# Kernel tuning notes

Hardware: AMD Instinct MI355X
Metric: run time of the kernel (lower is better)

Reference implementation:

```python
import jax, jax.numpy as jnp
import numpy as np

T_STEPS = 128
N_RAYS = 16384
RAY_EXT = 10.0  # ray_ext_factor


def _posenc(x, n_freq=4):
    # x: (...,3) in [-1,1] -> (...,3 + 3*2*n_freq) = (...,27)
    feats = [x]
    for k in range(n_freq):
        f = (2.0 ** k) * jnp.pi
        feats.append(jnp.sin(f * x))
        feats.append(jnp.cos(f * x))
    return jnp.concatenate(feats, -1)


def _sh_deg2(d):
    # real spherical harmonics, degree 0 and 1 (4 coeffs), d unit vectors (...,3)
    x, y, z = d[..., 0], d[..., 1], d[..., 2]
    c0 = 0.28209479177387814
    c1 = 0.4886025119029199
    return jnp.stack([jnp.full_like(x, c0), c1 * y, c1 * z, c1 * x], -1)


def _forward(rays_o, rays_d, tnoise, aabb, W1, b1, W2, b2, Wc1, bc1, Wc2, bc2):
    # --- ray-AABB intersection (slab method), RayBundle.intersect_aabb ---
    inv_d = 1.0 / rays_d
    t0 = (aabb[0] - rays_o) * inv_d
    t1 = (aabb[1] - rays_o) * inv_d
    tnear = jnp.maximum(jnp.max(jnp.minimum(t0, t1), -1, keepdims=True), 0.0)  # (N,1)
    tfar = jnp.min(jnp.maximum(t0, t1), -1, keepdims=True)                      # (N,1)
    active = (tfar > tnear).astype(rays_o.dtype)  # active_mask; masking replaces compaction

    # --- StratifiedRayStepSampler: ts (T,N,1) ---
    T = tnoise.shape[0]
    base = (jnp.arange(T, dtype=rays_o.dtype)[:, None, None] + tnoise) / T
    ts = tnear[None] + (tfar - tnear)[None] * base
    xyz = rays_o[None] + ts * rays_d[None]  # (T,N,3)

    # --- vol.sample(xyz, ynm, return_color=True): density + color MLP ---
    xn = 2.0 * (xyz - aabb[0]) / (aabb[1] - aabb[0]) - 1.0
    enc = _posenc(xn)                             # (T,N,27)
    h = jax.nn.relu(enc @ W1 + b1)                # (T,N,64)
    dh = h @ W2 + b2                              # (T,N,16)
    sigma = jnp.exp(dh[..., :1])                  # (T,N,1) density
    feat = dh[..., 1:]                            # (T,N,15)
    dnorm = jnp.linalg.norm(rays_d, axis=-1, keepdims=True)  # (N,1)
    ynm = _sh_deg2(rays_d / dnorm)                # encode_raydir -> (N,4)
    ynm = jnp.broadcast_to(ynm[None], (T,) + ynm.shape)      # expand to (T,N,4)
    hc = jax.nn.relu(jnp.concatenate([feat, ynm], -1) @ Wc1 + bc1)
    rgb = jax.nn.sigmoid(hc @ Wc2 + bc2)          # (T,N,3)

    # --- integrate_timesteps: transmittance-weighted compositing ---
    tfinal = tfar * RAY_EXT
    delta = jnp.concatenate([ts[1:] - ts[:-1], tfinal[None] - ts[-1:]], 0)  # (T,N,1)
    sd = sigma * delta * dnorm[None]
    alpha = 1.0 - jnp.exp(-sd)
    trans = jnp.exp(-(jnp.cumsum(sd, 0) - sd))    # exclusive cumsum transmittance
    w = trans * alpha * active[None]              # (T,N,1); inactive rays -> zero maps

    color = jnp.sum(w * rgb, 0)                   # color_map  (N,3)
    alpha_map = jnp.sum(w, 0)                     # alpha_map  (N,1)
    return jnp.concatenate([color, alpha_map], -1)  # rgba (N,4)


def setup_inputs() -> dict:
    key = jax.random.key(0)
    ks = jax.random.split(key, 8)
    # origins on a sphere of radius 2.5 around the unit aabb, aimed at points inside it
    o = jax.random.normal(ks[0], (N_RAYS, 3), jnp.float32)
    o = 2.5 * o / jnp.linalg.norm(o, axis=-1, keepdims=True)
    tgt = jax.random.uniform(ks[1], (N_RAYS, 3), jnp.float32, -0.5, 0.5)
    d = tgt - o
    d = d / jnp.linalg.norm(d, axis=-1, keepdims=True)
    aabb = jnp.array([[-1.0, -1.0, -1.0], [1.0, 1.0, 1.0]], jnp.float32)
    tnoise = jax.random.uniform(ks[2], (T_STEPS, N_RAYS, 1), jnp.float32)
    s1, s2, s3, s4 = 27 ** -0.5, 64 ** -0.5, 19 ** -0.5, 64 ** -0.5
    return {
        'rays_o': o, 'rays_d': d, 'tnoise': tnoise, 'aabb': aabb,
        'W1': jax.random.normal(ks[3], (27, 64), jnp.float32) * s1,
        'b1': jnp.zeros((64,), jnp.float32),
        'W2': jax.random.normal(ks[4], (64, 16), jnp.float32) * (0.1 * s2),
        'b2': jnp.zeros((16,), jnp.float32),
        'Wc1': jax.random.normal(ks[5], (19, 64), jnp.float32) * s3,
        'bc1': jnp.zeros((64,), jnp.float32),
        'Wc2': jax.random.normal(ks[6], (64, 3), jnp.float32) * s4,
        'bc2': jnp.zeros((3,), jnp.float32),
    }


def reference(rays_o, rays_d, tnoise, aabb, W1, b1, W2, b2, Wc1, bc1, Wc2, bc2):
    return _forward(rays_o, rays_d, tnoise, aabb, W1, b1, W2, b2, Wc1, bc1, Wc2, bc2)
```

## Files before the change

### kernel.cpp

```cpp
#include <hip/hip_runtime.h>
#include <stdint.h>

#define N_RAYS  16384
#define T_STEPS 128
#define RPW   16
#define WAVES 8
#define TSEG  16

typedef _Float16 half8  __attribute__((ext_vector_type(8)));
typedef __fp16   fp16x2 __attribute__((ext_vector_type(2)));
typedef float    float4_ __attribute__((ext_vector_type(4)));
typedef uint32_t uint2_  __attribute__((ext_vector_type(2)));

#define H8_W1    0
#define H8_FUSED 256
#define H8_WC2   896
#define F32_CV   4096
#define F32_BC2  4416
#define F32_S0   4432

__device__ __forceinline__ uint32_t pk(float a, float b) {
    fp16x2 h = __builtin_amdgcn_cvt_pkrtz(a, b);
    return __builtin_bit_cast(uint32_t, h);
}
__device__ __forceinline__ uint32_t pkr(float a, float b) {
    fp16x2 h = __builtin_amdgcn_cvt_pkrtz(a, b);
    fp16x2 z = {(__fp16)0.f, (__fp16)0.f};
    fp16x2 m = __builtin_elementwise_max(h, z);
    return __builtin_bit_cast(uint32_t, m);
}

__global__ void prep_weights(const float* __restrict__ W1, const float* __restrict__ b1,
                             const float* __restrict__ W2, const float* __restrict__ b2,
                             const float* __restrict__ Wc1, const float* __restrict__ bc1,
                             const float* __restrict__ Wc2, const float* __restrict__ bc2,
                             void* __restrict__ ws) {
    _Float16* wh = (_Float16*)ws;
    float*    wf = (float*)ws;
    int frag = blockIdx.x;
    int lane = threadIdx.x;
    int mm = lane & 15, q = lane >> 4;
    if (frag < 4) {
        int tau = frag;
        int n = tau * 16 + mm;
        for (int j = 0; j < 8; ++j) {
            float w;
            if (j < 6)      w = W1[(3 + 6 * q + j) * 64 + n];
            else if (j == 6) w = (q == 0) ? W1[0 * 64 + n] : (q == 1) ? W1[2 * 64 + n] : 0.f;
            else             w = (q == 0) ? W1[1 * 64 + n] : (q == 1) ? b1[n] : 0.f;
            wh[(H8_W1 + tau * 64 + lane) * 8 + j] = (_Float16)w;
        }
    } else if (frag < 14) {
        int f = frag - 4;
        int tau = f >> 1, kap = f & 1;
        int n_out = tau * 16 + mm;
        for (int j = 0; j < 8; ++j) {
            int k = kap * 32 + q * 8 + j;
            float w = 0.f;
            if (n_out < 64) {
                for (int c = 0; c < 15; ++c)
                    w += W2[k * 16 + 1 + c] * Wc1[c * 64 + n_out];
            } else if (n_out == 64) {
                w = W2[k * 16 + 0];
            }
            wh[(H8_FUSED + f * 64 + lane) * 8 + j] = (_Float16)w;
        }
    } else {
        int kap = frag - 14;
        for (int j = 0; j < 8; ++j) {
            int k = kap * 32 + q * 8 + j;
            wh[(H8_WC2 + kap * 64 + lane) * 8 + j] =
                (_Float16)((mm < 3) ? Wc2[k * 3 + mm] : 0.f);
        }
        if (frag == 15) {
            int n = lane;
            wf[F32_CV + 0 * 64 + n] = Wc1[15 * 64 + n];
            wf[F32_CV + 1 * 64 + n] = Wc1[16 * 64 + n];
            wf[F32_CV + 2 * 64 + n] = Wc1[17 * 64 + n];
            wf[F32_CV + 3 * 64 + n] = Wc1[18 * 64 + n];
            float cc = bc1[n];
            for (int c = 0; c < 15; ++c) cc += b2[1 + c] * Wc1[c * 64 + n];
            wf[F32_CV + 4 * 64 + n] = cc;
            if (lane < 16) wf[F32_BC2 + lane] = (lane < 3) ? bc2[lane] : 0.f;
            if (lane == 0) wf[F32_S0] = b2[0];
        }
    }
}

__global__ __launch_bounds__(512, 3)
void render_kernel(const float* __restrict__ rays_o, const float* __restrict__ rays_d,
                   const float* __restrict__ tnoise, const float* __restrict__ aabb,
                   const void* __restrict__ ws, float* __restrict__ out) {
    __shared__ __align__(16) _Float16 sH[WAVES][2][1024];
    __shared__ float sComb[WAVES][RPW][5];

    const int tid  = threadIdx.x;
    const int wv   = tid >> 6;
    const int lane = tid & 63;
    const int m    = lane & 15;
    const int q    = lane >> 4;
    const int r    = blockIdx.x * RPW + m;

    const half8* wsv = (const half8*)ws;
    const float* wsf = (const float*)ws;
    half8 fW1[4], fF[10], fWc2[2];
    #pragma unroll
    for (int i = 0; i < 4; ++i)  fW1[i]  = wsv[H8_W1    + i * 64 + lane];
    #pragma unroll
    for (int i = 0; i < 10; ++i) fF[i]   = wsv[H8_FUSED + i * 64 + lane];
    #pragma unroll
    for (int i = 0; i < 2; ++i)  fWc2[i] = wsv[H8_WC2   + i * 64 + lane];
    const float4_ binit = ((const float4_*)(wsf + F32_BC2))[q];
    const float s0b = wsf[F32_S0];

    float o0 = rays_o[r * 3 + 0], o1 = rays_o[r * 3 + 1], o2 = rays_o[r * 3 + 2];
    float d0 = rays_d[r * 3 + 0], d1 = rays_d[r * 3 + 1], d2 = rays_d[r * 3 + 2];
    float a00 = aabb[0], a01 = aabb[1], a02 = aabb[2];
    float a10 = aabb[3], a11 = aabb[4], a12 = aabb[5];

    float i0 = 1.0f / d0, i1 = 1.0f / d1, i2 = 1.0f / d2;
    float u0 = (a00 - o0) * i0, v0 = (a10 - o0) * i0;
    float u1 = (a01 - o1) * i1, v1 = (a11 - o1) * i1;
    float u2 = (a02 - o2) * i2, v2 = (a12 - o2) * i2;
    float tnear = fmaxf(fmaxf(fmaxf(fminf(u0, v0), fminf(u1, v1)), fminf(u2, v2)), 0.0f);
    float tfar  = fminf(fminf(fmaxf(u0, v0), fmaxf(u1, v1)), fmaxf(u2, v2));
    bool active = (tfar > tnear);
    float dt = tfar - tnear;
    float dt128 = dt * (1.0f / 128.0f);

    float dn  = sqrtf(d0 * d0 + d1 * d1 + d2 * d2);
    float idn = 1.0f / dn;
    const float c0sh = 0.28209479177387814f;
    const float c1sh = 0.4886025119029199f;
    float y1 = c1sh * d1 * idn, y2 = c1sh * d2 * idn, y3 = c1sh * d0 * idn;

    float4_ cv[4];
    #pragma unroll
    for (int tau = 0; tau < 4; ++tau) {
        #pragma unroll
        for (int reg = 0; reg < 4; ++reg) {
            int n = tau * 16 + 4 * q + reg;
            float c = wsf[F32_CV + 4 * 64 + n];
            c = fmaf(c0sh, wsf[F32_CV + 0 * 64 + n], c);
            c = fmaf(y1,   wsf[F32_CV + 1 * 64 + n], c);
            c = fmaf(y2,   wsf[F32_CV + 2 * 64 + n], c);
            c = fmaf(y3,   wsf[F32_CV + 3 * 64 + n], c);
            cv[tau][reg] = c;
        }
    }
    const float4_ c4init = {s0b, s0b, s0b, s0b};

    float qs = 0.5f * (float)(1 << q);
    float sc0 = 2.0f / (a10 - a00), of0 = -a00 * sc0 - 1.0f;
    float sc1 = 2.0f / (a11 - a01), of1 = -a01 * sc1 - 1.0f;
    float sc2 = 2.0f / (a12 - a02), of2 = -a02 * sc2 - 1.0f;
    float scq0 = sc0 * qs, ofq0 = of0 * qs;
    float scq1 = sc1 * qs, ofq1 = of1 * qs;
    float scq2 = sc2 * qs, ofq2 = of2 * qs;

    _Float16*       hwp[2];
    const _Float16* hrp[2];
    #pragma unroll
    for (int p = 0; p < 2; ++p) {
        hwp[p] = &sH[wv][p][((q >> 1) * 16 + m) * 8 + 4 * (q & 1)];
        hrp[p] = &sH[wv][p][(q * 16 + m) * 8];
    }

    const float4_ z4 = {0.f, 0.f, 0.f, 0.f};
    const bool q0 = (q == 0), q1 = (q == 1);

    float trans = 1.0f, sdtot = 0.0f, wacc = 0.0f;
    float cacc0 = 0.0f, cacc1 = 0.0f, cacc2 = 0.0f;

    const int tbase = wv * TSEG;
    float nA = tnoise[(tbase + 0) * N_RAYS + r];
    float nB = tnoise[(tbase + 1) * N_RAYS + r];

    #pragma unroll 1
    for (int tt = 0; tt < TSEG; tt += 2) {
        const int t0 = tbase + tt, t1 = t0 + 1;
        float nC = (t0 + 2 < T_STEPS) ? tnoise[(t0 + 2) * N_RAYS + r] : 0.0f;
        float nD = (t0 + 3 < T_STEPS) ? tnoise[(t0 + 3) * N_RAYS + r] : 0.0f;
        float ts0 = fmaf((float)t0 + nA, dt128, tnear);
        float ts1 = fmaf((float)t1 + nB, dt128, tnear);
        float ts2 = fmaf((float)(t0 + 2) + nC, dt128, tnear);
        float tsP[2] = {ts0, ts1};
        float deltaP[2];
        deltaP[0] = ts1 - ts0;
        deltaP[1] = (t1 < T_STEPS - 1) ? (ts2 - ts1) : fmaf(tfar, 10.0f, -ts1);
        nA = nC; nB = nD;

        float dhx[2];
        float4_ rgbP[2];

        #pragma unroll
        for (int p = 0; p < 2; ++p) {
            float x = fmaf(tsP[p], d0, o0);
            float y = fmaf(tsP[p], d1, o1);
            float z = fmaf(tsP[p], d2, o2);
            float xr0 = fmaf(x, scq0, ofq0);
            float xr1 = fmaf(y, scq1, ofq1);
            float xr2 = fmaf(z, scq2, ofq2);
            float s0 = __builtin_amdgcn_sinf(xr0);
            float s1 = __builtin_amdgcn_sinf(xr1);
            float s2 = __builtin_amdgcn_sinf(xr2);
            float cA = __builtin_amdgcn_cosf(xr0);
            float cB = __builtin_amdgcn_cosf(xr1);
            float cC = __builtin_amdgcn_cosf(xr2);
            float e6 = q0 ? (xr0 + xr0) : (q1 ? xr2 : 0.0f);
            float e7 = q0 ? (xr1 + xr1) : (q1 ? 1.0f : 0.0f);
            union { uint32_t u[4]; half8 h; } xf_;
            xf_.u[0] = pk(s0, s1); xf_.u[1] = pk(s2, cA);
            xf_.u[2] = pk(cB, cC); xf_.u[3] = pk(e6, e7);
            half8 xf = xf_.h;

            float4_ h0 = __builtin_amdgcn_mfma_f32_16x16x32_f16(fW1[0], xf, z4, 0, 0, 0);
            float4_ h1 = __builtin_amdgcn_mfma_f32_16x16x32_f16(fW1[1], xf, z4, 0, 0, 0);
            float4_ h2 = __builtin_amdgcn_mfma_f32_16x16x32_f16(fW1[2], xf, z4, 0, 0, 0);
            float4_ h3 = __builtin_amdgcn_mfma_f32_16x16x32_f16(fW1[3], xf, z4, 0, 0, 0);
            uint2_ w;
            w.x = pkr(h0.x, h0.y); w.y = pkr(h0.z, h0.w); *(uint2_*)(hwp[p] + 0 * 256) = w;
            w.x = pkr(h1.x, h1.y); w.y = pkr(h1.z, h1.w); *(uint2_*)(hwp[p] + 1 * 256) = w;
            w.x = pkr(h2.x, h2.y); w.y = pkr(h2.z, h2.w); *(uint2_*)(hwp[p] + 2 * 256) = w;
            w.x = pkr(h3.x, h3.y); w.y = pkr(h3.z, h3.w); *(uint2_*)(hwp[p] + 3 * 256) = w;
        }

        #pragma unroll
        for (int p = 0; p < 2; ++p) {
            half8 hb0 = *(const half8*)(hrp[p] + 0);
            half8 hb1 = *(const half8*)(hrp[p] + 512);
            float4_ d4 = __builtin_amdgcn_mfma_f32_16x16x32_f16(fF[8], hb0, c4init, 0, 0, 0);
            d4 = __builtin_amdgcn_mfma_f32_16x16x32_f16(fF[9], hb1, d4, 0, 0, 0);
            dhx[p] = d4.x;
            float4_ t0v = __builtin_amdgcn_mfma_f32_16x16x32_f16(fF[0], hb0, cv[0], 0, 0, 0);
            t0v = __builtin_amdgcn_mfma_f32_16x16x32_f16(fF[1], hb1, t0v, 0, 0, 0);
            float4_ t1v = __builtin_amdgcn_mfma_f32_16x16x32_f16(fF[2], hb0, cv[1], 0, 0, 0);
            t1v = __builtin_amdgcn_mfma_f32_16x16x32_f16(fF[3], hb1, t1v, 0, 0, 0);
            float4_ t2v = __builtin_amdgcn_mfma_f32_16x16x32_f16(fF[4], hb0, cv[2], 0, 0, 0);
            t2v = __builtin_amdgcn_mfma_f32_16x16x32_f16(fF[5], hb1, t2v, 0, 0, 0);
            float4_ t3v = __builtin_amdgcn_mfma_f32_16x16x32_f16(fF[6], hb0, cv[3], 0, 0, 0);
            t3v = __builtin_amdgcn_mfma_f32_16x16x32_f16(fF[7], hb1, t3v, 0, 0, 0);
            uint2_ w;
            w.x = pkr(t0v.x, t0v.y); w.y = pkr(t0v.z, t0v.w); *(uint2_*)(hwp[p] + 0 * 256) = w;
            w.x = pkr(t1v.x, t1v.y); w.y = pkr(t1v.z, t1v.w); *(uint2_*)(hwp[p] + 1 * 256) = w;
            w.x = pkr(t2v.x, t2v.y); w.y = pkr(t2v.z, t2v.w); *(uint2_*)(hwp[p] + 2 * 256) = w;
            w.x = pkr(t3v.x, t3v.y); w.y = pkr(t3v.z, t3v.w); *(uint2_*)(hwp[p] + 3 * 256) = w;
        }

        #pragma unroll
        for (int p = 0; p < 2; ++p) {
            half8 cb0 = *(const half8*)(hrp[p] + 0);
            half8 cb1 = *(const half8*)(hrp[p] + 512);
            float4_ rgbp = __builtin_amdgcn_mfma_f32_16x16x32_f16(fWc2[0], cb0, binit, 0, 0, 0);
            rgbP[p] = __builtin_amdgcn_mfma_f32_16x16x32_f16(fWc2[1], cb1, rgbp, 0, 0, 0);
        }

        if (q == 0) {
            #pragma unroll
            for (int p = 0; p < 2; ++p) {
                float sigma = __expf(dhx[p]);
                float sd = sigma * deltaP[p] * dn;
                float e = __expf(-sd);
                float alpha = 1.0f - e;
                float w = trans * alpha;
                float rr = __builtin_amdgcn_rcpf(1.0f + __expf(-rgbP[p].x));
                float rg = __builtin_amdgcn_rcpf(1.0f + __expf(-rgbP[p].y));
                float rb = __builtin_amdgcn_rcpf(1.0f + __expf(-rgbP[p].z));
                cacc0 = fmaf(w, rr, cacc0);
                cacc1 = fmaf(w, rg, cacc1);
                cacc2 = fmaf(w, rb, cacc2);
                wacc += w;
                trans *= e;
                sdtot += sd;
            }
        }
    }

    if (q == 0) {
        sComb[wv][m][0] = sdtot;
        sComb[wv][m][1] = wacc;
        sComb[wv][m][2] = cacc0;
        sComb[wv][m][3] = cacc1;
        sComb[wv][m][4] = cacc2;
    }
    __syncthreads();

    if (tid < RPW) {
        float P = 1.0f, C0 = 0.0f, C1 = 0.0f, C2 = 0.0f, WS = 0.0f;
        #pragma unroll
        for (int s = 0; s < WAVES; ++s) {
            C0 = fmaf(P, sComb[s][tid][2], C0);
            C1 = fmaf(P, sComb[s][tid][3], C1);
            C2 = fmaf(P, sComb[s][tid][4], C2);
            WS = fmaf(P, sComb[s][tid][1], WS);
            P *= __expf(-sComb[s][tid][0]);
        }
        float act = active ? 1.0f : 0.0f;
        const int rg = blockIdx.x * RPW + tid;
        out[rg * 4 + 0] = C0 * act;
        out[rg * 4 + 1] = C1 * act;
        out[rg * 4 + 2] = C2 * act;
        out[rg * 4 + 3] = WS * act;
    }
}

extern "C" void kernel_launch(void* const* d_in, const int* in_sizes, int n_in,
                              void* d_out, int out_size, void* d_ws, size_t ws_size,
                              hipStream_t stream) {
    const float* rays_o = (const float*)d_in[0];
    const float* rays_d = (const float*)d_in[1];
    const float* tnoise = (const float*)d_in[2];
    const float* aabb   = (const float*)d_in[3];
    const float* W1  = (const float*)d_in[4];
    const float* b1  = (const float*)d_in[5];
    const float* W2  = (const float*)d_in[6];
    const float* b2  = (const float*)d_in[7];
    const float* Wc1 = (const float*)d_in[8];
    const float* bc1 = (const float*)d_in[9];
    const float* Wc2 = (const float*)d_in[10];
    const float* bc2 = (const float*)d_in[11];

    prep_weights<<<dim3(16), dim3(64), 0, stream>>>(W1, b1, W2, b2, Wc1, bc1, Wc2, bc2, d_ws);

    dim3 grid(N_RAYS / RPW);
    dim3 block(WAVES * 64);
    render_kernel<<<grid, block, 0, stream>>>(rays_o, rays_d, tnoise, aabb, d_ws,
                                              (float*)d_out);
}
```

Measured before the change: 139.1 us.

## Unfuse W2·Wc1 product into W2 MFMA plus K16 color MFMA, halve waves

Replaces the precomputed fused W2·Wc1 weight (ten 16x16x32 MFMAs per step pair) with a true two-layer path: two 16x16x32 MFMAs compute the 16-wide dh, which is packed to fp16 and fed to four 16x16x16 MFMAs against Wc1. Lane k=0 of the Wc1 fragment is zeroed so the density channel is ignored. The density bias b2[0] is now added before exp instead of via the accumulator init. Block size drops to 4 waves with 32-step segments per wave, and launch bounds change to 256 threads with 4 blocks. This trims MFMA work and register pressure, at the cost of an extra fp16 rounding of dh and a serial dependency between the two matmuls.

```diff
diff --git a/kernel.cpp b/kernel.cpp
--- a/kernel.cpp
+++ b/kernel.cpp
@@ -4,20 +4,22 @@
 #define N_RAYS  16384
 #define T_STEPS 128
 #define RPW   16
-#define WAVES 8
-#define TSEG  16
+#define WAVES 4
+#define TSEG  32
 
 typedef _Float16 half8  __attribute__((ext_vector_type(8)));
+typedef _Float16 half4  __attribute__((ext_vector_type(4)));
 typedef __fp16   fp16x2 __attribute__((ext_vector_type(2)));
 typedef float    float4_ __attribute__((ext_vector_type(4)));
 typedef uint32_t uint2_  __attribute__((ext_vector_type(2)));
 
 #define H8_W1    0
-#define H8_FUSED 256
-#define H8_WC2   896
-#define F32_CV   4096
-#define F32_BC2  4416
-#define F32_S0   4432
+#define H8_W2    256
+#define H8_WC2   384
+#define H_WC1K16 4096
+#define F32_CV   3072
+#define F32_BC2  3392
+#define F32_S0   3408
 
 __device__ __forceinline__ uint32_t pk(float a, float b) {
     fp16x2 h = __builtin_amdgcn_cvt_pkrtz(a, b);
@@ -50,44 +52,42 @@
             else             w = (q == 0) ? W1[1 * 64 + n] : (q == 1) ? b1[n] : 0.f;
             wh[(H8_W1 + tau * 64 + lane) * 8 + j] = (_Float16)w;
         }
-    } else if (frag < 14) {
-        int f = frag - 4;
-        int tau = f >> 1, kap = f & 1;
-        int n_out = tau * 16 + mm;
+    } else if (frag < 6) {
+        int kap = frag - 4;
         for (int j = 0; j < 8; ++j) {
             int k = kap * 32 + q * 8 + j;
-            float w = 0.f;
-            if (n_out < 64) {
-                for (int c = 0; c < 15; ++c)
-                    w += W2[k * 16 + 1 + c] * Wc1[c * 64 + n_out];
-            } else if (n_out == 64) {
-                w = W2[k * 16 + 0];
-            }
-            wh[(H8_FUSED + f * 64 + lane) * 8 + j] = (_Float16)w;
-        }
-    } else {
-        int kap = frag - 14;
+            wh[(H8_W2 + kap * 64 + lane) * 8 + j] = (_Float16)W2[k * 16 + mm];
+        }
+    } else if (frag < 10) {
+        int tau = frag - 6;
+        int n2 = tau * 16 + mm;
+        for (int j = 0; j < 4; ++j) {
+            int k = 4 * q + j;
+            float w = (k == 0) ? 0.f : Wc1[(k - 1) * 64 + n2];
+            wh[H_WC1K16 + (tau * 64 + lane) * 4 + j] = (_Float16)w;
+        }
+    } else if (frag < 12) {
+        int kap = frag - 10;
         for (int j = 0; j < 8; ++j) {
             int k = kap * 32 + q * 8 + j;
             wh[(H8_WC2 + kap * 64 + lane) * 8 + j] =
                 (_Float16)((mm < 3) ? Wc2[k * 3 + mm] : 0.f);
         }
-        if (frag == 15) {
-            int n = lane;
-            wf[F32_CV + 0 * 64 + n] = Wc1[15 * 64 + n];
-            wf[F32_CV + 1 * 64 + n] = Wc1[16 * 64 + n];
-            wf[F32_CV + 2 * 64 + n] = Wc1[17 * 64 + n];
-            wf[F32_CV + 3 * 64 + n] = Wc1[18 * 64 + n];
-            float cc = bc1[n];
-            for (int c = 0; c < 15; ++c) cc += b2[1 + c] * Wc1[c * 64 + n];
-            wf[F32_CV + 4 * 64 + n] = cc;
-            if (lane < 16) wf[F32_BC2 + lane] = (lane < 3) ? bc2[lane] : 0.f;
-            if (lane == 0) wf[F32_S0] = b2[0];
-        }
-    }
-}
-
-__global__ __launch_bounds__(512, 3)
+    } else {
+        int n = lane;
+        wf[F32_CV + 0 * 64 + n] = Wc1[15 * 64 + n];
+        wf[F32_CV + 1 * 64 + n] = Wc1[16 * 64 + n];
+        wf[F32_CV + 2 * 64 + n] = Wc1[17 * 64 + n];
+        wf[F32_CV + 3 * 64 + n] = Wc1[18 * 64 + n];
+        float cc = bc1[n];
+        for (int c = 0; c < 15; ++c) cc += b2[1 + c] * Wc1[c * 64 + n];
+        wf[F32_CV + 4 * 64 + n] = cc;
+        if (lane < 16) wf[F32_BC2 + lane] = (lane < 3) ? bc2[lane] : 0.f;
+        if (lane == 0) wf[F32_S0] = b2[0];
+    }
+}
+
+__global__ __launch_bounds__(256, 4)
 void render_kernel(const float* __restrict__ rays_o, const float* __restrict__ rays_d,
                    const float* __restrict__ tnoise, const float* __restrict__ aabb,
                    const void* __restrict__ ws, float* __restrict__ out) {
@@ -101,15 +101,19 @@
     const int q    = lane >> 4;
     const int r    = blockIdx.x * RPW + m;
 
-    const half8* wsv = (const half8*)ws;
-    const float* wsf = (const float*)ws;
-    half8 fW1[4], fF[10], fWc2[2];
-    #pragma unroll
-    for (int i = 0; i < 4; ++i)  fW1[i]  = wsv[H8_W1    + i * 64 + lane];
-    #pragma unroll
-    for (int i = 0; i < 10; ++i) fF[i]   = wsv[H8_FUSED + i * 64 + lane];
-    #pragma unroll
-    for (int i = 0; i < 2; ++i)  fWc2[i] = wsv[H8_WC2   + i * 64 + lane];
+    const half8* wsv  = (const half8*)ws;
+    const half4* wsv4 = (const half4*)((const _Float16*)ws + H_WC1K16);
+    const float* wsf  = (const float*)ws;
+    half8 fW1[4], fW2[2], fWc2[2];
+    half4 fWc1[4];
+    #pragma unroll
+    for (int i = 0; i < 4; ++i) fW1[i]  = wsv[H8_W1  + i * 64 + lane];
+    #pragma unroll
+    for (int i = 0; i < 2; ++i) fW2[i]  = wsv[H8_W2  + i * 64 + lane];
+    #pragma unroll
+    for (int i = 0; i < 2; ++i) fWc2[i] = wsv[H8_WC2 + i * 64 + lane];
+    #pragma unroll
+    for (int i = 0; i < 4; ++i) fWc1[i] = wsv4[i * 64 + lane];
     const float4_ binit = ((const float4_*)(wsf + F32_BC2))[q];
     const float s0b = wsf[F32_S0];
 
@@ -148,7 +152,6 @@
             cv[tau][reg] = c;
         }
     }
-    const float4_ c4init = {s0b, s0b, s0b, s0b};
 
     float qs = 0.5f * (float)(1 << q);
     float sc0 = 2.0f / (a10 - a00), of0 = -a00 * sc0 - 1.0f;
@@ -229,17 +232,18 @@
         for (int p = 0; p < 2; ++p) {
             half8 hb0 = *(const half8*)(hrp[p] + 0);
             half8 hb1 = *(const half8*)(hrp[p] + 512);
-            float4_ d4 = __builtin_amdgcn_mfma_f32_16x16x32_f16(fF[8], hb0, c4init, 0, 0, 0);
-            d4 = __builtin_amdgcn_mfma_f32_16x16x32_f16(fF[9], hb1, d4, 0, 0, 0);
-            dhx[p] = d4.x;
-            float4_ t0v = __builtin_amdgcn_mfma_f32_16x16x32_f16(fF[0], hb0, cv[0], 0, 0, 0);
-            t0v = __builtin_amdgcn_mfma_f32_16x16x32_f16(fF[1], hb1, t0v, 0, 0, 0);
-            float4_ t1v = __builtin_amdgcn_mfma_f32_16x16x32_f16(fF[2], hb0, cv[1], 0, 0, 0);
-            t1v = __builtin_amdgcn_mfma_f32_16x16x32_f16(fF[3], hb1, t1v, 0, 0, 0);
-            float4_ t2v = __builtin_amdgcn_mfma_f32_16x16x32_f16(fF[4], hb0, cv[2], 0, 0, 0);
-            t2v = __builtin_amdgcn_mfma_f32_16x16x32_f16(fF[5], hb1, t2v, 0, 0, 0);
-            float4_ t3v = __builtin_amdgcn_mfma_f32_16x16x32_f16(fF[6], hb0, cv[3], 0, 0, 0);
-            t3v = __builtin_amdgcn_mfma_f32_16x16x32_f16(fF[7], hb1, t3v, 0, 0, 0);
+            float4_ dh = __builtin_amdgcn_mfma_f32_16x16x32_f16(fW2[0], hb0, z4, 0, 0, 0);
+            dh = __builtin_amdgcn_mfma_f32_16x16x32_f16(fW2[1], hb1, dh, 0, 0, 0);
+            dhx[p] = dh.x;
+
+            union { uint32_t u[2]; half4 h; } bf_;
+            bf_.u[0] = pk(dh.x, dh.y); bf_.u[1] = pk(dh.z, dh.w);
+            half4 fb = bf_.h;
+
+            float4_ t0v = __builtin_amdgcn_mfma_f32_16x16x16f16(fWc1[0], fb, cv[0], 0, 0, 0);
+            float4_ t1v = __builtin_amdgcn_mfma_f32_16x16x16f16(fWc1[1], fb, cv[1], 0, 0, 0);
+            float4_ t2v = __builtin_amdgcn_mfma_f32_16x16x16f16(fWc1[2], fb, cv[2], 0, 0, 0);
+            float4_ t3v = __builtin_amdgcn_mfma_f32_16x16x16f16(fWc1[3], fb, cv[3], 0, 0, 0);
             uint2_ w;
             w.x = pkr(t0v.x, t0v.y); w.y = pkr(t0v.z, t0v.w); *(uint2_*)(hwp[p] + 0 * 256) = w;
             w.x = pkr(t1v.x, t1v.y); w.y = pkr(t1v.z, t1v.w); *(uint2_*)(hwp[p] + 1 * 256) = w;
@@ -258,7 +262,7 @@
         if (q == 0) {
             #pragma unroll
             for (int p = 0; p < 2; ++p) {
-                float sigma = __expf(dhx[p]);
+                float sigma = __expf(dhx[p] + s0b);
                 float sd = sigma * deltaP[p] * dn;
                 float e = __expf(-sd);
                 float alpha = 1.0f - e;
@@ -320,7 +324,7 @@
     const float* Wc2 = (const float*)d_in[10];
     const float* bc2 = (const float*)d_in[11];
 
-    prep_weights<<<dim3(16), dim3(64), 0, stream>>>(W1, b1, W2, b2, Wc1, bc1, Wc2, bc2, d_ws);
+    prep_weights<<<dim3(13), dim3(64), 0, stream>>>(W1, b1, W2, b2, Wc1, bc1, Wc2, bc2, d_ws);
 
     dim3 grid(N_RAYS / RPW);
     dim3 block(WAVES * 64);
```

After: 120.9 us. -13.1%, faster.
